# Performance work log

Measured on AMD Instinct MI355X. Metric: run time of the kernel, lower is better.

Reference implementation:

```python
import jax, jax.numpy as jnp
import numpy as np
from jax import lax

DIM = 768
HEADS = 12
EXPERTS = 4
CAPS = [0.4, 0.3, 0.2, 0.1]  # capacity fraction per expert e=0..E-1 (e=E-1 is the full-dim expert)
EPS = 1e-5


def _layernorm(x, g, b):
    mu = jnp.mean(x, axis=-1, keepdims=True)
    var = jnp.mean(jnp.square(x - mu), axis=-1, keepdims=True)
    return (x - mu) * lax.rsqrt(var + EPS) * g + b


def _route(x, router_w, router_b):
    # Expert-preferred capacity router: experts (largest dim first) greedily take
    # their top-capacity tokens by router probability among still-unassigned tokens.
    B, N, _ = x.shape
    probs = jax.nn.softmax(x @ router_w + router_b, axis=-1)  # [B,N,E]
    ks = [int(c * N) for c in CAPS]
    ks[-1] += N - sum(ks)  # remainder to the largest expert
    assigned = jnp.zeros((B, N), dtype=jnp.int32)
    avail = jnp.ones((B, N), dtype=bool)
    brow = jnp.arange(B)[:, None]
    for e in reversed(range(EXPERTS)):
        pe = jnp.where(avail, probs[:, :, e], -jnp.inf)
        _, idx = lax.top_k(pe, ks[e])  # [B, k_e]
        sel = jnp.zeros((B, N), dtype=bool).at[brow, idx].set(True)
        assigned = jnp.where(sel, e, assigned)
        avail = avail & ~sel
    router_probs = jnp.take_along_axis(probs, assigned[..., None], axis=-1)[..., 0]  # [B,N]
    return assigned, router_probs


def _feat_mask(token_mask, dtype):
    # expert e uses the first DIM / 2^(E-1-e) features (nested slicing)
    dims = jnp.array([DIM >> (EXPERTS - 1 - e) for e in range(EXPERTS)], dtype=jnp.int32)
    d_tok = dims[token_mask]  # [B,N]
    return (jnp.arange(DIM)[None, None, :] < d_tok[..., None]).astype(dtype)  # [B,N,D]


def _nested_attention(h, mask, wqkv, bqkv, wo, bo):
    # masking input + output of a full projection == using the top-left nested submatrix
    B, N, D = h.shape
    hd = D // HEADS
    qkv = ((h * mask) @ wqkv + bqkv) * jnp.tile(mask, (1, 1, 3))  # [B,N,3D]
    q, k, v = jnp.split(qkv, 3, axis=-1)
    q = q.reshape(B, N, HEADS, hd).transpose(0, 2, 1, 3)  # [B,H,N,hd]
    k = k.reshape(B, N, HEADS, hd).transpose(0, 2, 1, 3)
    v = v.reshape(B, N, HEADS, hd).transpose(0, 2, 1, 3)
    scores = jnp.einsum('bhqd,bhkd->bhqk', q, k) * (hd ** -0.5)
    attn = jax.nn.softmax(scores, axis=-1)
    out = jnp.einsum('bhqk,bhkd->bhqd', attn, v)  # [B,H,N,hd]
    out = out.transpose(0, 2, 1, 3).reshape(B, N, D) * mask
    return ((out @ wo) + bo) * mask


def setup_inputs() -> dict:
    key = jax.random.key(0)
    ks = jax.random.split(key, 8)
    B, N, D = 4, 1024, DIM
    s = 0.02
    return {
        'x': jax.random.normal(ks[0], (B, N, D), jnp.float32),
        'ln1_g': jnp.ones((D,), jnp.float32),
        'ln1_b': jnp.zeros((D,), jnp.float32),
        'router_w': jax.random.normal(ks[1], (D, EXPERTS), jnp.float32) * s,
        'router_b': jnp.zeros((EXPERTS,), jnp.float32),
        'wqkv': jax.random.normal(ks[2], (D, 3 * D), jnp.float32) * s,
        'bqkv': jnp.zeros((3 * D,), jnp.float32),
        'wo': jax.random.normal(ks[3], (D, D), jnp.float32) * s,
        'bo': jnp.zeros((D,), jnp.float32),
        'ln2_g': jnp.ones((D,), jnp.float32),
        'ln2_b': jnp.zeros((D,), jnp.float32),
        'w1': jax.random.normal(ks[4], (D, 4 * D), jnp.float32) * s,
        'b1': jnp.zeros((4 * D,), jnp.float32),
        'w2': jax.random.normal(ks[5], (4 * D, D), jnp.float32) * s,
        'b2': jnp.zeros((D,), jnp.float32),
    }


def reference(x, ln1_g, ln1_b, router_w, router_b, wqkv, bqkv, wo, bo,
              ln2_g, ln2_b, w1, b1, w2, b2):
    token_mask, router_probs = _route(x, router_w, router_b)
    mask = _feat_mask(token_mask, x.dtype)  # [B,N,D]
    z = x + _nested_attention(_layernorm(x, ln1_g, ln1_b), mask, wqkv, bqkv, wo, bo)
    h2 = _layernorm(z, ln2_g, ln2_b)
    z_prime = jax.nn.gelu(h2 @ w1 + b1, approximate=False) @ w2 + b2
    # probability-weighted token combine
    return z + router_probs[..., None] * z_prime
```

## Files before the change

### kernel.cpp

```cpp
#include <hip/hip_runtime.h>
#include <math.h>

#define DIM 768
#define NTOK 1024
#define BATCH 4
#define HEADS 12
#define TOKENS (BATCH * NTOK)

typedef __bf16 bf16;
typedef __attribute__((ext_vector_type(8))) __bf16 bf16x8;
typedef __attribute__((ext_vector_type(4))) float floatx4;

__device__ __forceinline__ void async_ld16(const bf16* g, bf16* l) {
    __builtin_amdgcn_global_load_lds((const __attribute__((address_space(1))) unsigned int*)g,
                                     (__attribute__((address_space(3))) unsigned int*)l, 16, 0, 0);
}

__global__ void router_kernel(const float* __restrict__ x,
                              const float* __restrict__ rw,
                              const float* __restrict__ rb,
                              float* __restrict__ probs) {
    int t = blockIdx.x;
    int tid = threadIdx.x;
    const float* xr = x + (size_t)t * DIM;
    double acc[4] = {0, 0, 0, 0};
    for (int k = tid; k < DIM; k += 256) {
        double xv = (double)xr[k];
        acc[0] += xv * (double)rw[k * 4 + 0];
        acc[1] += xv * (double)rw[k * 4 + 1];
        acc[2] += xv * (double)rw[k * 4 + 2];
        acc[3] += xv * (double)rw[k * 4 + 3];
    }
    __shared__ double red[256];
    __shared__ double logits[4];
    for (int e = 0; e < 4; ++e) {
        red[tid] = acc[e];
        __syncthreads();
        for (int s = 128; s > 0; s >>= 1) {
            if (tid < s) red[tid] += red[tid + s];
            __syncthreads();
        }
        if (tid == 0) logits[e] = red[0] + (double)rb[e];
        __syncthreads();
    }
    if (tid == 0) {
        double m = logits[0];
        for (int e = 1; e < 4; ++e) m = fmax(m, logits[e]);
        double s = 0.0, p[4];
        for (int e = 0; e < 4; ++e) { p[e] = exp(logits[e] - m); s += p[e]; }
        for (int e = 0; e < 4; ++e) probs[(size_t)t * 4 + e] = (float)(p[e] / s);
    }
}

template <int E, int KCAP, bool FIRST, bool LAST>
__global__ __launch_bounds__(256) void route_pass(const float* __restrict__ probs,
                                                  int* __restrict__ avail,
                                                  int* __restrict__ dtok_g,
                                                  float* __restrict__ rprobs_g) {
    int b = blockIdx.y;
    int i = blockIdx.x * 256 + threadIdx.x;
    const float* pb = probs + (size_t)b * NTOK * 4;
    __shared__ float sp[1024];
    for (int j = threadIdx.x; j < 1024; j += 256) {
        bool av = FIRST ? true : (avail[b * NTOK + j] != 0);
        sp[j] = av ? pb[j * 4 + E] : -INFINITY;
    }
    __syncthreads();
    bool av_i = FIRST ? true : (avail[b * NTOK + i] != 0);
    float pi = sp[i];
    int cnt = 0;
#pragma unroll 8
    for (int j0 = 0; j0 < 1024; j0 += 4) {
        floatx4 pj = *(const floatx4*)&sp[j0];
        cnt += (pj[0] > pi) || (pj[0] == pi && (j0 + 0) < i);
        cnt += (pj[1] > pi) || (pj[1] == pi && (j0 + 1) < i);
        cnt += (pj[2] > pi) || (pj[2] == pi && (j0 + 2) < i);
        cnt += (pj[3] > pi) || (pj[3] == pi && (j0 + 3) < i);
    }
    bool sel = av_i && (cnt < KCAP);
    if (sel) {
        dtok_g[b * NTOK + i] = DIM >> (3 - E);
        rprobs_g[b * NTOK + i] = pb[i * 4 + E];
    } else if (LAST && av_i) {
        dtok_g[b * NTOK + i] = DIM >> 3;
        rprobs_g[b * NTOK + i] = pb[i * 4 + 0];
    }
    if (!LAST) {
        if (FIRST) avail[b * NTOK + i] = sel ? 0 : 1;
        else if (sel) avail[b * NTOK + i] = 0;
    }
}

__global__ void ln_mask_kernel(const float* __restrict__ x,
                               const float* __restrict__ g,
                               const float* __restrict__ bta,
                               const int* __restrict__ dtok,
                               bf16* __restrict__ out) {
    int t = blockIdx.x;
    int tid = threadIdx.x;
    const float* xr = x + (size_t)t * DIM;
    float s = 0.0f;
    for (int k = tid; k < DIM; k += 256) s += xr[k];
    __shared__ float red[256];
    red[tid] = s;
    __syncthreads();
    for (int st = 128; st > 0; st >>= 1) {
        if (tid < st) red[tid] += red[tid + st];
        __syncthreads();
    }
    float mu = red[0] / DIM;
    __syncthreads();
    float v = 0.0f;
    for (int k = tid; k < DIM; k += 256) { float d = xr[k] - mu; v += d * d; }
    red[tid] = v;
    __syncthreads();
    for (int st = 128; st > 0; st >>= 1) {
        if (tid < st) red[tid] += red[tid + st];
        __syncthreads();
    }
    float rs = rsqrtf(red[0] / DIM + 1e-5f);
    int d = dtok ? dtok[t] : DIM;
    for (int k = tid; k < DIM; k += 256) {
        float val = (xr[k] - mu) * rs * g[k] + bta[k];
        out[(size_t)t * DIM + k] = (bf16)((k < d) ? val : 0.0f);
    }
}

__global__ __launch_bounds__(256) void wo_ln2_kernel(const float* __restrict__ part,
                                                     const float* __restrict__ x,
                                                     const float* __restrict__ bo,
                                                     const int* __restrict__ dtok,
                                                     const float* __restrict__ g,
                                                     const float* __restrict__ bta,
                                                     float* __restrict__ z,
                                                     bf16* __restrict__ h2) {
    int t = blockIdx.x;
    int tid = threadIdx.x;
    int d = dtok[t];
    float vals[3];
    float s = 0.0f;
#pragma unroll
    for (int i = 0; i < 3; ++i) {
        int k = i * 256 + tid;
        float c = (k < d) ? (part[(size_t)t * DIM + k] +
                             part[(size_t)TOKENS * DIM + (size_t)t * DIM + k] + bo[k])
                          : 0.0f;
        c += x[(size_t)t * DIM + k];
        vals[i] = c;
        s += c;
    }
    __shared__ float red[256];
    red[tid] = s;
    __syncthreads();
    for (int st = 128; st > 0; st >>= 1) {
        if (tid < st) red[tid] += red[tid + st];
        __syncthreads();
    }
    float mu = red[0] / DIM;
    __syncthreads();
    float v = 0.0f;
#pragma unroll
    for (int i = 0; i < 3; ++i) { float dd = vals[i] - mu; v += dd * dd; }
    red[tid] = v;
    __syncthreads();
    for (int st = 128; st > 0; st >>= 1) {
        if (tid < st) red[tid] += red[tid + st];
        __syncthreads();
    }
    float rs = rsqrtf(red[0] / DIM + 1e-5f);
#pragma unroll
    for (int i = 0; i < 3; ++i) {
        int k = i * 256 + tid;
        z[(size_t)t * DIM + k] = vals[i];
        h2[(size_t)t * DIM + k] = (bf16)((vals[i] - mu) * rs * g[k] + bta[k]);
    }
}

__global__ __launch_bounds__(256) void transpose_bf16_kernel(const float* __restrict__ W,
                                                             bf16* __restrict__ Wt,
                                                             int K, int N) {
    __shared__ float t[32][33];
    int bx = blockIdx.x * 32;
    int by = blockIdx.y * 32;
    int tx = threadIdx.x, ty = threadIdx.y;
#pragma unroll
    for (int i = 0; i < 4; ++i)
        t[ty + i * 8][tx] = W[(size_t)(by + ty + i * 8) * N + bx + tx];
    __syncthreads();
#pragma unroll
    for (int i = 0; i < 4; ++i)
        Wt[(size_t)(bx + ty + i * 8) * K + by + tx] = (bf16)t[tx][ty + i * 8];
}

__global__ __launch_bounds__(256) void vt_trans_kernel(const bf16* __restrict__ qkv,
                                                       bf16* __restrict__ vtg) {
    int nt = blockIdx.x;
    int h = blockIdx.y;
    int b = blockIdx.z;
    int tid = threadIdx.x;
    __shared__ bf16 T[64 * 72];
    size_t base = (size_t)b * NTOK * 2304;
#pragma unroll
    for (int u = 0; u < 2; ++u) {
        int e = u * 256 + tid;
        int row = e >> 3, part = e & 7;
        *(floatx4*)&T[row * 72 + part * 8] =
            *(const floatx4*)&qkv[base + (size_t)(nt * 64 + row) * 2304 + 1536 + h * 64 + part * 8];
    }
    __syncthreads();
    size_t vbase = ((size_t)(b * HEADS + h)) * 64 * NTOK;
#pragma unroll
    for (int u = 0; u < 2; ++u) {
        int e = u * 256 + tid;
        int d = e >> 3, ng = e & 7;
        bf16 tmp[8];
#pragma unroll
        for (int j = 0; j < 8; ++j) tmp[j] = T[(ng * 8 + j) * 72 + d];
        *(floatx4*)&vtg[vbase + (size_t)d * NTOK + nt * 64 + ng * 8] = *(floatx4*)tmp;
    }
}

template <int MODE>
__global__ __launch_bounds__(256) void gemm_mfma(const bf16* __restrict__ A,
                                                 const bf16* __restrict__ Bt,
                                                 const float* __restrict__ bias,
                                                 void* __restrict__ Cout,
                                                 int M, int NN, int K, int Kc,
                                                 const int* __restrict__ dtok) {
    __shared__ bf16 As[128 * 32];
    __shared__ bf16 Bs[128 * 32];
    int n0 = blockIdx.x * 128;
    int m0 = blockIdx.y * 128;
    int kbase = blockIdx.z * Kc;
    int tid = threadIdx.x;
    int wv = tid >> 6;
    int lane = tid & 63;
    int l16 = lane & 15, q4 = lane >> 4;
    int wm = (wv >> 1) * 64, wn = (wv & 1) * 64;
    int srow = lane >> 2, scol = (lane & 3) * 8;
    const bf16* gA0 = A + (size_t)(m0 + 32 * wv + srow) * K + kbase + scol;
    const bf16* gB0 = Bt + (size_t)(n0 + 32 * wv + srow) * K + kbase + scol;
    const bf16* gA1 = gA0 + (size_t)16 * K;
    const bf16* gB1 = gB0 + (size_t)16 * K;
    bf16* lA0 = &As[(32 * wv) * 32];
    bf16* lA1 = &As[(32 * wv + 16) * 32];
    bf16* lB0 = &Bs[(32 * wv) * 32];
    bf16* lB1 = &Bs[(32 * wv + 16) * 32];
    floatx4 acc[4][4] = {};
    int kIters = Kc / 32;
    for (int it = 0; it < kIters; ++it) {
        __syncthreads();
        async_ld16(gA0, lA0);
        async_ld16(gA1, lA1);
        async_ld16(gB0, lB0);
        async_ld16(gB1, lB1);
        gA0 += 32; gA1 += 32; gB0 += 32; gB1 += 32;
        __syncthreads();
        bf16x8 af[4], bfr[4];
#pragma unroll
        for (int t = 0; t < 4; ++t) {
            af[t] = *(const bf16x8*)&As[(wm + t * 16 + l16) * 32 + q4 * 8];
            bfr[t] = *(const bf16x8*)&Bs[(wn + t * 16 + l16) * 32 + q4 * 8];
        }
#pragma unroll
        for (int i = 0; i < 4; ++i)
#pragma unroll
            for (int j = 0; j < 4; ++j)
                acc[i][j] = __builtin_amdgcn_mfma_f32_16x16x32_bf16(af[i], bfr[j], acc[i][j], 0, 0, 0);
    }
#pragma unroll
    for (int i = 0; i < 4; ++i) {
#pragma unroll
        for (int j = 0; j < 4; ++j) {
            int col = n0 + wn + j * 16 + l16;
#pragma unroll
            for (int r = 0; r < 4; ++r) {
                int row = m0 + wm + i * 16 + q4 * 4 + r;
                if (MODE == 4) {
                    ((float*)Cout)[(size_t)blockIdx.z * M * NN + (size_t)row * NN + col] =
                        acc[i][j][r];
                } else if (MODE == 0) {
                    float c = acc[i][j][r] + bias[col];
                    int jm = col % 768;
                    c = (jm < dtok[row]) ? c : 0.0f;
                    ((bf16*)Cout)[(size_t)row * NN + col] = (bf16)c;
                } else if (MODE == 2) {
                    float c = acc[i][j][r] + bias[col];
                    c = 0.5f * c * (1.0f + erff(c * 0.70710678118654752f));
                    ((bf16*)Cout)[(size_t)row * NN + col] = (bf16)c;
                }
            }
        }
    }
}

__global__ __launch_bounds__(256) void ffn2_reduce(const float* __restrict__ part,
                                                   const float* __restrict__ z,
                                                   const float* __restrict__ bias,
                                                   const float* __restrict__ rp,
                                                   float* __restrict__ out) {
    size_t idx = ((size_t)blockIdx.x * 256 + threadIdx.x) * 4;
    int row = (int)(idx / DIM);
    int col = (int)(idx % DIM);
    floatx4 p0 = *(const floatx4*)&part[idx];
    floatx4 p1 = *(const floatx4*)&part[(size_t)TOKENS * DIM + idx];
    floatx4 zz = *(const floatx4*)&z[idx];
    floatx4 bb = *(const floatx4*)&bias[col];
    float r = rp[row];
    floatx4 o = zz + (p0 + p1 + bb) * r;
    *(floatx4*)&out[idx] = o;
}

#define LDH 72
__global__ __launch_bounds__(256) void attn_mfma(const bf16* __restrict__ qkv,
                                                 const bf16* __restrict__ vtg,
                                                 const int* __restrict__ dtok,
                                                 bf16* __restrict__ attno) {
    int qt = blockIdx.x;
    int h = blockIdx.y;
    int b = blockIdx.z;
    int tid = threadIdx.x;
    int wv = tid >> 6;
    int lane = tid & 63;
    int l16 = lane & 15, q4 = lane >> 4;
    __shared__ bf16 Qs[64 * LDH];
    __shared__ bf16 Ks[64 * LDH];
    __shared__ bf16 Vt[64 * LDH];
    __shared__ bf16 Ps[4][16 * LDH];
    size_t base = (size_t)b * NTOK * 2304;
    size_t vbase = ((size_t)(b * HEADS + h)) * 64 * NTOK;
    int erow = tid >> 3, epart = tid & 7;
#pragma unroll
    for (int u = 0; u < 2; ++u) {
        int row = (u * 256 + tid) >> 3, part = (u * 256 + tid) & 7;
        *(floatx4*)&Qs[row * LDH + part * 8] =
            *(const floatx4*)&qkv[base + (size_t)(qt * 64 + row) * 2304 + h * 64 + part * 8];
    }
    floatx4 o[4] = {};
    float m_r[4] = {-INFINITY, -INFINITY, -INFINITY, -INFINITY};
    float l_r[4] = {0.0f, 0.0f, 0.0f, 0.0f};
    floatx4 kreg[2], vreg[2];
#pragma unroll
    for (int u = 0; u < 2; ++u) {
        int row = (u * 256 + tid) >> 3, part = (u * 256 + tid) & 7;
        kreg[u] = *(const floatx4*)&qkv[base + (size_t)row * 2304 + 768 + h * 64 + part * 8];
        vreg[u] = *(const floatx4*)&vtg[vbase + (size_t)row * NTOK + part * 8];
    }
    for (int kt = 0; kt < 16; ++kt) {
        __syncthreads();
#pragma unroll
        for (int u = 0; u < 2; ++u) {
            int row = (u * 256 + tid) >> 3, part = (u * 256 + tid) & 7;
            *(floatx4*)&Ks[row * LDH + part * 8] = kreg[u];
            *(floatx4*)&Vt[row * LDH + part * 8] = vreg[u];
        }
        __syncthreads();
        if (kt < 15) {
#pragma unroll
            for (int u = 0; u < 2; ++u) {
                int row = (u * 256 + tid) >> 3, part = (u * 256 + tid) & 7;
                kreg[u] = *(const floatx4*)&qkv[base + (size_t)((kt + 1) * 64 + row) * 2304 + 768 +
                                                h * 64 + part * 8];
                vreg[u] = *(const floatx4*)&vtg[vbase + (size_t)row * NTOK + (kt + 1) * 64 + part * 8];
            }
        }
        floatx4 sc[4] = {};
#pragma unroll
        for (int ch = 0; ch < 2; ++ch) {
            bf16x8 aq = *(const bf16x8*)&Qs[(wv * 16 + l16) * LDH + ch * 32 + q4 * 8];
#pragma unroll
            for (int nt = 0; nt < 4; ++nt) {
                bf16x8 bk = *(const bf16x8*)&Ks[(nt * 16 + l16) * LDH + ch * 32 + q4 * 8];
                sc[nt] = __builtin_amdgcn_mfma_f32_16x16x32_bf16(aq, bk, sc[nt], 0, 0, 0);
            }
        }
        float alpha[4], psum[4];
#pragma unroll
        for (int r = 0; r < 4; ++r) {
            float v0 = fmaxf(fmaxf(sc[0][r], sc[1][r]), fmaxf(sc[2][r], sc[3][r])) * 0.125f;
#pragma unroll
            for (int msk = 1; msk < 16; msk <<= 1) v0 = fmaxf(v0, __shfl_xor(v0, msk));
            float mn = fmaxf(m_r[r], v0);
            alpha[r] = __expf(m_r[r] - mn);
            m_r[r] = mn;
            psum[r] = 0.0f;
        }
#pragma unroll
        for (int nt = 0; nt < 4; ++nt)
#pragma unroll
            for (int r = 0; r < 4; ++r) {
                float p = __expf(sc[nt][r] * 0.125f - m_r[r]);
                psum[r] += p;
                Ps[wv][(q4 * 4 + r) * LDH + nt * 16 + l16] = (bf16)p;
            }
#pragma unroll
        for (int r = 0; r < 4; ++r) {
            float s = psum[r];
#pragma unroll
            for (int msk = 1; msk < 16; msk <<= 1) s += __shfl_xor(s, msk);
            l_r[r] = l_r[r] * alpha[r] + s;
        }
#pragma unroll
        for (int dt = 0; dt < 4; ++dt)
#pragma unroll
            for (int r = 0; r < 4; ++r) o[dt][r] *= alpha[r];
#pragma unroll
        for (int ch = 0; ch < 2; ++ch) {
            bf16x8 ap = *(const bf16x8*)&Ps[wv][l16 * LDH + ch * 32 + q4 * 8];
#pragma unroll
            for (int dt = 0; dt < 4; ++dt) {
                bf16x8 bv = *(const bf16x8*)&Vt[(dt * 16 + l16) * LDH + ch * 32 + q4 * 8];
                o[dt] = __builtin_amdgcn_mfma_f32_16x16x32_bf16(ap, bv, o[dt], 0, 0, 0);
            }
        }
    }
#pragma unroll
    for (int r = 0; r < 4; ++r) {
        int tokrow = qt * 64 + wv * 16 + q4 * 4 + r;
        int dt_tok = dtok[b * NTOK + tokrow];
        float inv = 1.0f / l_r[r];
#pragma unroll
        for (int dt = 0; dt < 4; ++dt) {
            int col = h * 64 + dt * 16 + l16;
            float val = (col < dt_tok) ? o[dt][r] * inv : 0.0f;
            attno[((size_t)b * NTOK + tokrow) * DIM + col] = (bf16)val;
        }
    }
    (void)erow; (void)epart;
}

extern "C" void kernel_launch(void* const* d_in, const int* in_sizes, int n_in,
                              void* d_out, int out_size, void* d_ws, size_t ws_size,
                              hipStream_t stream) {
    const float* x = (const float*)d_in[0];
    const float* ln1g = (const float*)d_in[1];
    const float* ln1b = (const float*)d_in[2];
    const float* rw = (const float*)d_in[3];
    const float* rb = (const float*)d_in[4];
    const float* wqkv = (const float*)d_in[5];
    const float* bqkv = (const float*)d_in[6];
    const float* wo = (const float*)d_in[7];
    const float* bo = (const float*)d_in[8];
    const float* ln2g = (const float*)d_in[9];
    const float* ln2b = (const float*)d_in[10];
    const float* w1 = (const float*)d_in[11];
    const float* b1 = (const float*)d_in[12];
    const float* w2 = (const float*)d_in[13];
    const float* b2 = (const float*)d_in[14];
    float* out = (float*)d_out;

    char* ws = (char*)d_ws;
    size_t off = 0;
    auto alloc = [&](size_t bytes) {
        void* p = ws + off;
        off = (off + bytes + 255) & ~(size_t)255;
        return p;
    };
    bf16* h1m = (bf16*)alloc(sizeof(bf16) * TOKENS * DIM);
    float* probs = (float*)alloc(sizeof(float) * TOKENS * 4);
    float* rprobs = (float*)alloc(sizeof(float) * TOKENS);
    int* dtok = (int*)alloc(sizeof(int) * TOKENS);
    int* avail = (int*)alloc(sizeof(int) * TOKENS);
    bf16* qkvb = (bf16*)alloc(sizeof(bf16) * TOKENS * 3 * DIM);
    bf16* vtg = (bf16*)alloc(sizeof(bf16) * BATCH * HEADS * 64 * NTOK);
    bf16* attno = (bf16*)alloc(sizeof(bf16) * TOKENS * DIM);
    float* z = (float*)alloc(sizeof(float) * TOKENS * DIM);
    bf16* h2 = (bf16*)alloc(sizeof(bf16) * TOKENS * DIM);
    bf16* ffn1 = (bf16*)alloc(sizeof(bf16) * TOKENS * 4 * DIM);
    bf16* wqkvT = (bf16*)alloc(sizeof(bf16) * DIM * 3 * DIM);
    bf16* woT = (bf16*)alloc(sizeof(bf16) * DIM * DIM);
    bf16* w1T = (bf16*)alloc(sizeof(bf16) * DIM * 4 * DIM);
    bf16* w2T = (bf16*)alloc(sizeof(bf16) * 4 * DIM * DIM);
    float* part = (float*)alloc(sizeof(float) * 2 * TOKENS * DIM);

    dim3 tb(32, 8);
    transpose_bf16_kernel<<<dim3(2304 / 32, 768 / 32), tb, 0, stream>>>(wqkv, wqkvT, 768, 2304);
    transpose_bf16_kernel<<<dim3(768 / 32, 768 / 32), tb, 0, stream>>>(wo, woT, 768, 768);
    transpose_bf16_kernel<<<dim3(3072 / 32, 768 / 32), tb, 0, stream>>>(w1, w1T, 768, 3072);
    transpose_bf16_kernel<<<dim3(768 / 32, 3072 / 32), tb, 0, stream>>>(w2, w2T, 3072, 768);

    router_kernel<<<TOKENS, 256, 0, stream>>>(x, rw, rb, probs);
    route_pass<3, 104, true, false><<<dim3(4, BATCH), 256, 0, stream>>>(probs, avail, dtok, rprobs);
    route_pass<2, 204, false, false><<<dim3(4, BATCH), 256, 0, stream>>>(probs, avail, dtok, rprobs);
    route_pass<1, 307, false, true><<<dim3(4, BATCH), 256, 0, stream>>>(probs, avail, dtok, rprobs);
    ln_mask_kernel<<<TOKENS, 256, 0, stream>>>(x, ln1g, ln1b, dtok, h1m);
    gemm_mfma<0><<<dim3(2304 / 128, 4096 / 128), 256, 0, stream>>>(
        h1m, wqkvT, bqkv, qkvb, TOKENS, 2304, 768, 768, dtok);
    vt_trans_kernel<<<dim3(16, HEADS, BATCH), 256, 0, stream>>>(qkvb, vtg);
    attn_mfma<<<dim3(16, HEADS, BATCH), 256, 0, stream>>>(qkvb, vtg, dtok, attno);
    gemm_mfma<4><<<dim3(768 / 128, 4096 / 128, 2), 256, 0, stream>>>(
        attno, woT, nullptr, part, TOKENS, 768, 768, 384, nullptr);
    wo_ln2_kernel<<<TOKENS, 256, 0, stream>>>(part, x, bo, dtok, ln2g, ln2b, z, h2);
    gemm_mfma<2><<<dim3(3072 / 128, 4096 / 128), 256, 0, stream>>>(
        h2, w1T, b1, ffn1, TOKENS, 3072, 768, 768, nullptr);
    gemm_mfma<4><<<dim3(768 / 128, 4096 / 128, 2), 256, 0, stream>>>(
        ffn1, w2T, nullptr, part, TOKENS, 768, 3072, 1536, nullptr);
    ffn2_reduce<<<TOKENS * DIM / 1024, 256, 0, stream>>>(part, z, b2, rprobs, out);
}
```

Baseline: 435.6 us.

## Double-buffer GEMM LDS tiles, swap grid order, fuse weight transposes

The GEMM now prefetches the next K-slab of A and B into a second LDS buffer while MFMAs run on the current one, leaving one barrier per iteration instead of two. The grid is reordered so blockIdx.x walks M tiles and blockIdx.y walks N tiles, which changes which blocks share weight tiles in cache. The four weight transpose launches become a single launch, cutting launch overhead. The risk is that the async LDS loads are not explicitly waited on before the barrier, so correctness depends on the barrier draining outstanding vmcnt, and LDS use doubles.

```diff
diff --git a/kernel.cpp b/kernel.cpp
--- a/kernel.cpp
+++ b/kernel.cpp
@@ -176,20 +176,32 @@
     }
 }
 
-__global__ __launch_bounds__(256) void transpose_bf16_kernel(const float* __restrict__ W,
-                                                             bf16* __restrict__ Wt,
-                                                             int K, int N) {
+__global__ __launch_bounds__(256) void transpose_all_kernel(const float* __restrict__ wqkv,
+                                                            const float* __restrict__ wo,
+                                                            const float* __restrict__ w1,
+                                                            const float* __restrict__ w2,
+                                                            bf16* __restrict__ o0,
+                                                            bf16* __restrict__ o1,
+                                                            bf16* __restrict__ o2,
+                                                            bf16* __restrict__ o3) {
+    int id = blockIdx.x;
+    const float* W;
+    bf16* Wt;
+    int K, N, bx, by;
+    if (id < 1728) { W = wqkv; Wt = o0; K = 768; N = 2304; bx = id % 72; by = id / 72; }
+    else if (id < 2304) { int r = id - 1728; W = wo; Wt = o1; K = 768; N = 768; bx = r % 24; by = r / 24; }
+    else if (id < 4608) { int r = id - 2304; W = w1; Wt = o2; K = 768; N = 3072; bx = r % 96; by = r / 96; }
+    else { int r = id - 4608; W = w2; Wt = o3; K = 3072; N = 768; bx = r % 24; by = r / 24; }
     __shared__ float t[32][33];
-    int bx = blockIdx.x * 32;
-    int by = blockIdx.y * 32;
-    int tx = threadIdx.x, ty = threadIdx.y;
+    int x0 = bx * 32, y0 = by * 32;
+    int tx = threadIdx.x & 31, ty = threadIdx.x >> 5;
 #pragma unroll
     for (int i = 0; i < 4; ++i)
-        t[ty + i * 8][tx] = W[(size_t)(by + ty + i * 8) * N + bx + tx];
+        t[ty + i * 8][tx] = W[(size_t)(y0 + ty + i * 8) * N + x0 + tx];
     __syncthreads();
 #pragma unroll
     for (int i = 0; i < 4; ++i)
-        Wt[(size_t)(bx + ty + i * 8) * K + by + tx] = (bf16)t[tx][ty + i * 8];
+        Wt[(size_t)(x0 + ty + i * 8) * K + y0 + tx] = (bf16)t[tx][ty + i * 8];
 }
 
 __global__ __launch_bounds__(256) void vt_trans_kernel(const bf16* __restrict__ qkv,
@@ -227,10 +239,10 @@
                                                  void* __restrict__ Cout,
                                                  int M, int NN, int K, int Kc,
                                                  const int* __restrict__ dtok) {
-    __shared__ bf16 As[128 * 32];
-    __shared__ bf16 Bs[128 * 32];
-    int n0 = blockIdx.x * 128;
-    int m0 = blockIdx.y * 128;
+    __shared__ bf16 As[2][128 * 32];
+    __shared__ bf16 Bs[2][128 * 32];
+    int m0 = blockIdx.x * 128;
+    int n0 = blockIdx.y * 128;
     int kbase = blockIdx.z * Kc;
     int tid = threadIdx.x;
     int wv = tid >> 6;
@@ -242,31 +254,37 @@
     const bf16* gB0 = Bt + (size_t)(n0 + 32 * wv + srow) * K + kbase + scol;
     const bf16* gA1 = gA0 + (size_t)16 * K;
     const bf16* gB1 = gB0 + (size_t)16 * K;
-    bf16* lA0 = &As[(32 * wv) * 32];
-    bf16* lA1 = &As[(32 * wv + 16) * 32];
-    bf16* lB0 = &Bs[(32 * wv) * 32];
-    bf16* lB1 = &Bs[(32 * wv + 16) * 32];
+    int o0 = (32 * wv) * 32, o1 = (32 * wv + 16) * 32;
+    async_ld16(gA0, &As[0][o0]);
+    async_ld16(gA1, &As[0][o1]);
+    async_ld16(gB0, &Bs[0][o0]);
+    async_ld16(gB1, &Bs[0][o1]);
+    gA0 += 32; gA1 += 32; gB0 += 32; gB1 += 32;
+    __syncthreads();
     floatx4 acc[4][4] = {};
     int kIters = Kc / 32;
+    int cur = 0;
     for (int it = 0; it < kIters; ++it) {
-        __syncthreads();
-        async_ld16(gA0, lA0);
-        async_ld16(gA1, lA1);
-        async_ld16(gB0, lB0);
-        async_ld16(gB1, lB1);
-        gA0 += 32; gA1 += 32; gB0 += 32; gB1 += 32;
-        __syncthreads();
+        if (it + 1 < kIters) {
+            async_ld16(gA0, &As[cur ^ 1][o0]);
+            async_ld16(gA1, &As[cur ^ 1][o1]);
+            async_ld16(gB0, &Bs[cur ^ 1][o0]);
+            async_ld16(gB1, &Bs[cur ^ 1][o1]);
+            gA0 += 32; gA1 += 32; gB0 += 32; gB1 += 32;
+        }
         bf16x8 af[4], bfr[4];
 #pragma unroll
         for (int t = 0; t < 4; ++t) {
-            af[t] = *(const bf16x8*)&As[(wm + t * 16 + l16) * 32 + q4 * 8];
-            bfr[t] = *(const bf16x8*)&Bs[(wn + t * 16 + l16) * 32 + q4 * 8];
+            af[t] = *(const bf16x8*)&As[cur][(wm + t * 16 + l16) * 32 + q4 * 8];
+            bfr[t] = *(const bf16x8*)&Bs[cur][(wn + t * 16 + l16) * 32 + q4 * 8];
         }
 #pragma unroll
         for (int i = 0; i < 4; ++i)
 #pragma unroll
             for (int j = 0; j < 4; ++j)
                 acc[i][j] = __builtin_amdgcn_mfma_f32_16x16x32_bf16(af[i], bfr[j], acc[i][j], 0, 0, 0);
+        __syncthreads();
+        cur ^= 1;
     }
 #pragma unroll
     for (int i = 0; i < 4; ++i) {
@@ -329,7 +347,6 @@
     __shared__ bf16 Ps[4][16 * LDH];
     size_t base = (size_t)b * NTOK * 2304;
     size_t vbase = ((size_t)(b * HEADS + h)) * 64 * NTOK;
-    int erow = tid >> 3, epart = tid & 7;
 #pragma unroll
     for (int u = 0; u < 2; ++u) {
         int row = (u * 256 + tid) >> 3, part = (u * 256 + tid) & 7;
@@ -426,7 +443,6 @@
             attno[((size_t)b * NTOK + tokrow) * DIM + col] = (bf16)val;
         }
     }
-    (void)erow; (void)epart;
 }
 
 extern "C" void kernel_launch(void* const* d_in, const int* in_sizes, int n_in,
@@ -473,27 +489,23 @@
     bf16* w2T = (bf16*)alloc(sizeof(bf16) * 4 * DIM * DIM);
     float* part = (float*)alloc(sizeof(float) * 2 * TOKENS * DIM);
 
-    dim3 tb(32, 8);
-    transpose_bf16_kernel<<<dim3(2304 / 32, 768 / 32), tb, 0, stream>>>(wqkv, wqkvT, 768, 2304);
-    transpose_bf16_kernel<<<dim3(768 / 32, 768 / 32), tb, 0, stream>>>(wo, woT, 768, 768);
-    transpose_bf16_kernel<<<dim3(3072 / 32, 768 / 32), tb, 0, stream>>>(w1, w1T, 768, 3072);
-    transpose_bf16_kernel<<<dim3(768 / 32, 3072 / 32), tb, 0, stream>>>(w2, w2T, 3072, 768);
+    transpose_all_kernel<<<6912, 256, 0, stream>>>(wqkv, wo, w1, w2, wqkvT, woT, w1T, w2T);
 
     router_kernel<<<TOKENS, 256, 0, stream>>>(x, rw, rb, probs);
     route_pass<3, 104, true, false><<<dim3(4, BATCH), 256, 0, stream>>>(probs, avail, dtok, rprobs);
     route_pass<2, 204, false, false><<<dim3(4, BATCH), 256, 0, stream>>>(probs, avail, dtok, rprobs);
     route_pass<1, 307, false, true><<<dim3(4, BATCH), 256, 0, stream>>>(probs, avail, dtok, rprobs);
     ln_mask_kernel<<<TOKENS, 256, 0, stream>>>(x, ln1g, ln1b, dtok, h1m);
-    gemm_mfma<0><<<dim3(2304 / 128, 4096 / 128), 256, 0, stream>>>(
+    gemm_mfma<0><<<dim3(4096 / 128, 2304 / 128), 256, 0, stream>>>(
         h1m, wqkvT, bqkv, qkvb, TOKENS, 2304, 768, 768, dtok);
     vt_trans_kernel<<<dim3(16, HEADS, BATCH), 256, 0, stream>>>(qkvb, vtg);
     attn_mfma<<<dim3(16, HEADS, BATCH), 256, 0, stream>>>(qkvb, vtg, dtok, attno);
-    gemm_mfma<4><<<dim3(768 / 128, 4096 / 128, 2), 256, 0, stream>>>(
+    gemm_mfma<4><<<dim3(4096 / 128, 768 / 128, 2), 256, 0, stream>>>(
         attno, woT, nullptr, part, TOKENS, 768, 768, 384, nullptr);
     wo_ln2_kernel<<<TOKENS, 256, 0, stream>>>(part, x, bo, dtok, ln2g, ln2b, z, h2);
-    gemm_mfma<2><<<dim3(3072 / 128, 4096 / 128), 256, 0, stream>>>(
+    gemm_mfma<2><<<dim3(4096 / 128, 3072 / 128), 256, 0, stream>>>(
         h2, w1T, b1, ffn1, TOKENS, 3072, 768, 768, nullptr);
-    gemm_mfma<4><<<dim3(768 / 128, 4096 / 128, 2), 256, 0, stream>>>(
+    gemm_mfma<4><<<dim3(4096 / 128, 768 / 128, 2), 256, 0, stream>>>(
         ffn1, w2T, nullptr, part, TOKENS, 768, 3072, 1536, nullptr);
     ffn2_reduce<<<TOKENS * DIM / 1024, 256, 0, stream>>>(part, z, b2, rprobs, out);
 }
```

Measured after the change: 409.5 us. 1.06x faster.
